# Optimization experiments

Measured on AMD Instinct MI355X. Metric: run time of the kernel, lower is better.

The kernel has to match this reference:

```python
import jax, jax.numpy as jnp
import numpy as np

DELTA = 0.2
TOPK = 10
RECALL_KS = (1, 5, 10)


def setup_inputs() -> dict:
    key = jax.random.key(0)
    k1, k2 = jax.random.split(key)
    B, D = 8192, 256
    x = jax.random.normal(k1, (B, D), dtype=jnp.float32)
    y = jax.random.normal(k2, (B, D), dtype=jnp.float32)
    return {"x": x, "y": y}


def reference(x, y):
    B = x.shape[0]
    # L2-normalize rows (matches x / sqrt(sum(x*x), keepdim))
    xn = x / jnp.sqrt(jnp.sum(x * x, axis=1, keepdims=True))
    yn = y / jnp.sqrt(jnp.sum(y * y, axis=1, keepdims=True))
    sim = xn @ yn.T                      # [B, B]
    diag = jnp.diagonal(sim)             # [B]
    cor = diag[:, None]                  # cor_similarity[i, j] = sim[i, i]
    loss_mat = jnp.maximum(0.0, sim - cor + DELTA) + jnp.maximum(0.0, sim.T - cor + DELTA)
    # zero the diagonal (vectorized version of the python loop)
    loss_mat = loss_mat * (1.0 - jnp.eye(B, dtype=loss_mat.dtype))
    loss = jnp.sum(loss_mat) / B

    # metrics (no grad in original)
    score = sim - cor                    # [B, B]
    _, pred = jax.lax.top_k(score, TOPK)  # [B, 10] indices, descending
    # torch code: pred.t() [10,B] eq arange(B); equivalent untransposed:
    correct = pred == jnp.arange(B)[:, None]          # [B, 10]
    correct_per_rank = jnp.sum(correct, axis=0)        # [10] hits at rank j
    recall = jnp.stack([jnp.sum(correct[:, :k]) for k in RECALL_KS]).astype(jnp.int32)
    # ndcg weight ln(2)/ln(2+j) for rank j (0-based), matching math.log(2)/math.log(2+j)
    w = jnp.log(2.0) / jnp.log(2.0 + jnp.arange(TOPK, dtype=jnp.float32))
    ndcg = jnp.stack([jnp.sum(correct_per_rank[:k].astype(jnp.float32) * w[:k]) for k in RECALL_KS])
    return loss, recall, ndcg
```

## Files before the change

### kernel.cpp

```cpp
#include <hip/hip_runtime.h>
#include <math.h>

#define NB 8192
#define ND 256
#define DELTA_F 0.2f

typedef __attribute__((ext_vector_type(8))) __bf16 bf16x8;
typedef __attribute__((ext_vector_type(4))) __bf16 bf16x4;
typedef __attribute__((ext_vector_type(4))) float f32x4;

__device__ __forceinline__ void gload16(const void* g, void* l) {
  __builtin_amdgcn_global_load_lds(
      (const __attribute__((address_space(1))) void*)g,
      (__attribute__((address_space(3))) void*)l, 16, 0, 0);
}

__global__ __launch_bounds__(256) void normalize_split_k(
    const float* __restrict__ x, const float* __restrict__ y,
    __bf16* __restrict__ Xh, __bf16* __restrict__ Xl,
    __bf16* __restrict__ Yh, __bf16* __restrict__ Yl,
    float* __restrict__ dd) {
  const int w = threadIdx.x >> 6, lane = threadIdx.x & 63;
  const int i = blockIdx.x * 4 + w;
  const size_t rbase = (size_t)i * ND;
  const float4 xv = *(const float4*)&x[rbase + lane * 4];
  const float4 yv = *(const float4*)&y[rbase + lane * 4];
  float sxx = xv.x * xv.x + xv.y * xv.y + xv.z * xv.z + xv.w * xv.w;
  float syy = yv.x * yv.x + yv.y * yv.y + yv.z * yv.z + yv.w * yv.w;
  float sxy = xv.x * yv.x + xv.y * yv.y + xv.z * yv.z + xv.w * yv.w;
#pragma unroll
  for (int o = 1; o < 64; o <<= 1) {
    sxx += __shfl_xor(sxx, o, 64);
    syy += __shfl_xor(syy, o, 64);
    sxy += __shfl_xor(sxy, o, 64);
  }
  const float ix = 1.0f / sqrtf(sxx);
  const float iy = 1.0f / sqrtf(syy);
  if (lane == 0) dd[i] = sxy * ix * iy;

  const float xs[4] = {xv.x * ix, xv.y * ix, xv.z * ix, xv.w * ix};
  const float ys[4] = {yv.x * iy, yv.y * iy, yv.z * iy, yv.w * iy};
  bf16x4 xh, xl, yh, yl;
#pragma unroll
  for (int e = 0; e < 4; ++e) {
    const __bf16 h = (__bf16)xs[e];
    xh[e] = h; xl[e] = (__bf16)(xs[e] - (float)h);
    const __bf16 g = (__bf16)ys[e];
    yh[e] = g; yl[e] = (__bf16)(ys[e] - (float)g);
  }
  *(bf16x4*)&Xh[rbase + lane * 4] = xh;
  *(bf16x4*)&Xl[rbase + lane * 4] = xl;
  *(bf16x4*)&Yh[rbase + lane * 4] = yh;
  *(bf16x4*)&Yl[rbase + lane * 4] = yl;
}

__global__ __launch_bounds__(256) void gemm_mfma(
    const __bf16* __restrict__ Xh, const __bf16* __restrict__ Xl,
    const __bf16* __restrict__ Yh, const __bf16* __restrict__ Yl,
    const float* __restrict__ dd,
    float* __restrict__ loss_accum, int* __restrict__ cnt) {
  __shared__ __bf16 sT[4][128][32];
  __shared__ int c_loc[128];
  __shared__ float lred[4];

  const int tid = threadIdx.x;
  const int lin = blockIdx.y * 64 + blockIdx.x;
  const int swz = (lin & 7) * 512 + (lin >> 3);
  const int bi = swz >> 6, bj = swz & 63;
  const int row0 = bi * 128, col0 = bj * 128;

  const int lane = tid & 63, wid = tid >> 6;
  const int wr = wid >> 1, wc = wid & 1;
  const int lr = lane & 15, lkc = lane >> 4;

  for (int r = tid; r < 128; r += 256) c_loc[r] = 0;

  const __bf16* msrc = (wid == 0) ? Xh : (wid == 1) ? Xl : (wid == 2) ? Yh : Yl;
  const int mbase = (wid < 2) ? row0 : col0;
  const int sr = lane >> 2, sc = lane & 3;
  const int ssw = sc ^ ((sr >> 1) & 3);
  const char* gp[8];
#pragma unroll
  for (int i = 0; i < 8; ++i)
    gp[i] = (const char*)msrc + (size_t)(mbase + i * 16 + sr) * (ND * 2) + ssw * 16;
  __bf16* const lbase = &sT[wid][0][0];

  f32x4 acc[4][4];
#pragma unroll
  for (int m = 0; m < 4; ++m)
#pragma unroll
    for (int n = 0; n < 4; ++n) acc[m][n] = (f32x4)(0.0f);

  const int arow = wr * 64 + lr;
  const int bcol = wc * 64 + lr;
  const int cko = (lkc ^ ((lr >> 1) & 3)) * 8;

#pragma unroll
  for (int k0 = 0; k0 < ND; k0 += 32) {
    __syncthreads();
#pragma unroll
    for (int i = 0; i < 8; ++i)
      gload16(gp[i] + k0 * 2, lbase + i * 512);
    __syncthreads();

    bf16x8 ah[4], al[4], bh[4], bl[4];
#pragma unroll
    for (int m = 0; m < 4; ++m) {
      ah[m] = *(const bf16x8*)&sT[0][arow + m * 16][cko];
      al[m] = *(const bf16x8*)&sT[1][arow + m * 16][cko];
    }
#pragma unroll
    for (int n = 0; n < 4; ++n) {
      bh[n] = *(const bf16x8*)&sT[2][bcol + n * 16][cko];
      bl[n] = *(const bf16x8*)&sT[3][bcol + n * 16][cko];
    }
#pragma unroll
    for (int m = 0; m < 4; ++m)
#pragma unroll
      for (int n = 0; n < 4; ++n) {
        acc[m][n] = __builtin_amdgcn_mfma_f32_16x16x32_bf16(ah[m], bh[n], acc[m][n], 0, 0, 0);
        acc[m][n] = __builtin_amdgcn_mfma_f32_16x16x32_bf16(ah[m], bl[n], acc[m][n], 0, 0, 0);
        acc[m][n] = __builtin_amdgcn_mfma_f32_16x16x32_bf16(al[m], bh[n], acc[m][n], 0, 0, 0);
      }
  }

  float djv[4];
#pragma unroll
  for (int n = 0; n < 4; ++n) djv[n] = dd[col0 + wc * 64 + n * 16 + lr];

  float lsum = 0.f;
#pragma unroll
  for (int m = 0; m < 4; ++m) {
    const int rbase = wr * 64 + m * 16 + lkc * 4;
#pragma unroll
    for (int q = 0; q < 4; ++q) {
      const int gi = row0 + rbase + q;
      const float dival = dd[gi];
      int cl = 0;
#pragma unroll
      for (int n = 0; n < 4; ++n) {
        const int gj = col0 + wc * 64 + n * 16 + lr;
        const float s = acc[m][n][q];
        if (gi != gj) {
          lsum += fmaxf(0.f, s - dival + DELTA_F) + fmaxf(0.f, s - djv[n] + DELTA_F);
          cl += (s > dival) ? 1 : 0;
        }
      }
      cl += __shfl_xor(cl, 1, 64);
      cl += __shfl_xor(cl, 2, 64);
      cl += __shfl_xor(cl, 4, 64);
      cl += __shfl_xor(cl, 8, 64);
      if (lr == 0) atomicAdd(&c_loc[rbase + q], cl);
    }
  }

#pragma unroll
  for (int o = 32; o > 0; o >>= 1) lsum += __shfl_down(lsum, o, 64);
  if (lane == 0) lred[wid] = lsum;
  __syncthreads();
  if (tid == 0) atomicAdd(loss_accum, lred[0] + lred[1] + lred[2] + lred[3]);
  if (tid < 128) atomicAdd(&cnt[row0 + tid], c_loc[tid]);
}

__global__ __launch_bounds__(256) void finalize_k(
    const float* __restrict__ loss_accum, const int* __restrict__ cnt,
    float* __restrict__ out) {
  const int t = threadIdx.x;
  float a6[6] = {0.f, 0.f, 0.f, 0.f, 0.f, 0.f};
  for (int i = t; i < NB; i += 256) {
    const int c = cnt[i];
    if (c < 10) {
      const float w = 0.69314718055994531f / logf(2.0f + (float)c);
      a6[2] += 1.f; a6[5] += w;
      if (c < 5) { a6[1] += 1.f; a6[4] += w; }
      if (c < 1) { a6[0] += 1.f; a6[3] += w; }
    }
  }
  __shared__ float red[6][4];
#pragma unroll
  for (int j = 0; j < 6; ++j) {
    float v = a6[j];
#pragma unroll
    for (int o = 32; o > 0; o >>= 1) v += __shfl_down(v, o, 64);
    if ((t & 63) == 0) red[j][t >> 6] = v;
  }
  __syncthreads();
  if (t == 0) {
    out[0] = loss_accum[0] / (float)NB;
#pragma unroll
    for (int j = 0; j < 6; ++j)
      out[1 + j] = red[j][0] + red[j][1] + red[j][2] + red[j][3];
  }
}

extern "C" void kernel_launch(void* const* d_in, const int* in_sizes, int n_in,
                              void* d_out, int out_size, void* d_ws, size_t ws_size,
                              hipStream_t stream) {
  const float* x = (const float*)d_in[0];
  const float* y = (const float*)d_in[1];
  float* out = (float*)d_out;

  char* ws = (char*)d_ws;
  float* loss_accum = (float*)ws;
  int* cnt = (int*)(ws + 256);
  float* dd = (float*)(ws + 256 + 32768);

  const size_t splitOff = 256 + 2 * 32768;
  const size_t matB = (size_t)NB * ND * 2;
  __bf16* Xh = (__bf16*)(ws + splitOff);
  __bf16* Xl = (__bf16*)(ws + splitOff + matB);
  __bf16* Yh = (__bf16*)(ws + splitOff + 2 * matB);
  __bf16* Yl = (__bf16*)(ws + splitOff + 3 * matB);

  hipMemsetAsync(ws, 0, 256 + 32768, stream);
  hipLaunchKernelGGL(normalize_split_k, dim3(NB / 4), dim3(256), 0, stream,
                     x, y, Xh, Xl, Yh, Yl, dd);
  hipLaunchKernelGGL(gemm_mfma, dim3(64, 64), dim3(256), 0, stream,
                     Xh, Xl, Yh, Yl, dd, loss_accum, cnt);
  hipLaunchKernelGGL(finalize_k, dim3(1), dim3(256), 0, stream, loss_accum, cnt, out);
}
```

Baseline: 155.0 us.

## Use 256x256 tiles with a 4-stage pipelined LDS loop over the split-bf16 K

```diff
diff --git a/kernel.cpp b/kernel.cpp
--- a/kernel.cpp
+++ b/kernel.cpp
@@ -4,6 +4,7 @@
 #define NB 8192
 #define ND 256
 #define DELTA_F 0.2f
+#define NT 24
 
 typedef __attribute__((ext_vector_type(8))) __bf16 bf16x8;
 typedef __attribute__((ext_vector_type(4))) __bf16 bf16x4;
@@ -19,7 +20,7 @@
     const float* __restrict__ x, const float* __restrict__ y,
     __bf16* __restrict__ Xh, __bf16* __restrict__ Xl,
     __bf16* __restrict__ Yh, __bf16* __restrict__ Yl,
-    float* __restrict__ dd) {
+    float* __restrict__ dd, float* __restrict__ loss_accum, int* __restrict__ cnt) {
   const int w = threadIdx.x >> 6, lane = threadIdx.x & 63;
   const int i = blockIdx.x * 4 + w;
   const size_t rbase = (size_t)i * ND;
@@ -36,8 +37,11 @@
   }
   const float ix = 1.0f / sqrtf(sxx);
   const float iy = 1.0f / sqrtf(syy);
-  if (lane == 0) dd[i] = sxy * ix * iy;
-
+  if (lane == 0) {
+    dd[i] = sxy * ix * iy;
+    cnt[i] = 0;
+    if (i == 0) loss_accum[0] = 0.0f;
+  }
   const float xs[4] = {xv.x * ix, xv.y * ix, xv.z * ix, xv.w * ix};
   const float ys[4] = {yv.x * iy, yv.y * iy, yv.z * iy, yv.w * iy};
   bf16x4 xh, xl, yh, yl;
@@ -54,74 +58,89 @@
   *(bf16x4*)&Yl[rbase + lane * 4] = yl;
 }
 
-__global__ __launch_bounds__(256) void gemm_mfma(
+__global__ __launch_bounds__(512, 2) void gemm_mfma(
     const __bf16* __restrict__ Xh, const __bf16* __restrict__ Xl,
     const __bf16* __restrict__ Yh, const __bf16* __restrict__ Yl,
     const float* __restrict__ dd,
     float* __restrict__ loss_accum, int* __restrict__ cnt) {
-  __shared__ __bf16 sT[4][128][32];
-  __shared__ int c_loc[128];
-  __shared__ float lred[4];
+  __shared__ __bf16 sAB[4][2][256][32];
+  __shared__ int c_loc[256];
+  __shared__ float lred[8];
 
   const int tid = threadIdx.x;
-  const int lin = blockIdx.y * 64 + blockIdx.x;
-  const int swz = (lin & 7) * 512 + (lin >> 3);
-  const int bi = swz >> 6, bj = swz & 63;
-  const int row0 = bi * 128, col0 = bj * 128;
+  const int bid = blockIdx.x;
+  const int xcd = bid & 7, idx = bid >> 3;
+  const int bi = xcd * 4 + (idx & 3);
+  const int bj = (idx >> 5) * 8 + ((idx >> 2) & 7);
+  const int row0 = bi * 256, col0 = bj * 256;
 
   const int lane = tid & 63, wid = tid >> 6;
-  const int wr = wid >> 1, wc = wid & 1;
+  const int wr = wid >> 2, wc = wid & 3;
   const int lr = lane & 15, lkc = lane >> 4;
 
-  for (int r = tid; r < 128; r += 256) c_loc[r] = 0;
-
-  const __bf16* msrc = (wid == 0) ? Xh : (wid == 1) ? Xl : (wid == 2) ? Yh : Yl;
-  const int mbase = (wid < 2) ? row0 : col0;
-  const int sr = lane >> 2, sc = lane & 3;
-  const int ssw = sc ^ ((sr >> 1) & 3);
-  const char* gp[8];
-#pragma unroll
-  for (int i = 0; i < 8; ++i)
-    gp[i] = (const char*)msrc + (size_t)(mbase + i * 16 + sr) * (ND * 2) + ssw * 16;
-  __bf16* const lbase = &sT[wid][0][0];
-
-  f32x4 acc[4][4];
-#pragma unroll
-  for (int m = 0; m < 4; ++m)
+  if (tid < 256) c_loc[tid] = 0;
+
+  const int rowl = tid >> 2;
+  const int swz = (tid & 3) ^ ((tid >> 3) & 3);
+  const size_t offA0 = (size_t)(row0 + rowl) * (ND * 2) + swz * 16;
+  const size_t offB0 = (size_t)(col0 + rowl) * (ND * 2) + swz * 16;
+  char* const lds0 = (char*)&sAB[0][0][0][0];
+
+  f32x4 acc[8][4];
+#pragma unroll
+  for (int m = 0; m < 8; ++m)
 #pragma unroll
     for (int n = 0; n < 4; ++n) acc[m][n] = (f32x4)(0.0f);
 
-  const int arow = wr * 64 + lr;
-  const int bcol = wc * 64 + lr;
+  auto stage = [&](int t) {
+    const char* pa = (const char*)((t >= 8 && t < 16) ? Xl : Xh) + (t & 7) * 64;
+    const char* pb = (const char*)((t >= 16) ? Yl : Yh) + (t & 7) * 64;
+    char* lb = lds0 + (t & 3) * 32768;
+    gload16(pa + offA0,         lb + tid * 16);
+    gload16(pa + offA0 + 65536, lb + 8192 + tid * 16);
+    gload16(pb + offB0,         lb + 16384 + tid * 16);
+    gload16(pb + offB0 + 65536, lb + 24576 + tid * 16);
+  };
+
   const int cko = (lkc ^ ((lr >> 1) & 3)) * 8;
-
-#pragma unroll
-  for (int k0 = 0; k0 < ND; k0 += 32) {
-    __syncthreads();
-#pragma unroll
-    for (int i = 0; i < 8; ++i)
-      gload16(gp[i] + k0 * 2, lbase + i * 512);
-    __syncthreads();
-
-    bf16x8 ah[4], al[4], bh[4], bl[4];
-#pragma unroll
-    for (int m = 0; m < 4; ++m) {
-      ah[m] = *(const bf16x8*)&sT[0][arow + m * 16][cko];
-      al[m] = *(const bf16x8*)&sT[1][arow + m * 16][cko];
-    }
-#pragma unroll
-    for (int n = 0; n < 4; ++n) {
-      bh[n] = *(const bf16x8*)&sT[2][bcol + n * 16][cko];
-      bl[n] = *(const bf16x8*)&sT[3][bcol + n * 16][cko];
-    }
+  const int arow = wr * 128 + lr;
+  const int brow = wc * 64 + lr;
+
+#pragma unroll
+  for (int t = 0; t < 3; ++t) stage(t);
+
+#pragma unroll
+  for (int t = 0; t < NT; ++t) {
+    if (t + 3 < NT) stage(t + 3);
+    __builtin_amdgcn_sched_barrier(0);
+    if (t < NT - 3)       asm volatile("s_waitcnt vmcnt(12)\n\ts_barrier" ::: "memory");
+    else if (t == NT - 3) asm volatile("s_waitcnt vmcnt(8)\n\ts_barrier" ::: "memory");
+    else if (t == NT - 2) asm volatile("s_waitcnt vmcnt(4)\n\ts_barrier" ::: "memory");
+    else                  asm volatile("s_waitcnt vmcnt(0)\n\ts_barrier" ::: "memory");
+
+    const int b = t & 3;
+    bf16x8 bf[4], af[8];
+#pragma unroll
+    for (int n = 0; n < 4; ++n) bf[n] = *(const bf16x8*)&sAB[b][1][brow + n * 16][cko];
+#pragma unroll
+    for (int m = 0; m < 8; ++m) af[m] = *(const bf16x8*)&sAB[b][0][arow + m * 16][cko];
+
+    __builtin_amdgcn_s_setprio(1);
 #pragma unroll
     for (int m = 0; m < 4; ++m)
 #pragma unroll
-      for (int n = 0; n < 4; ++n) {
-        acc[m][n] = __builtin_amdgcn_mfma_f32_16x16x32_bf16(ah[m], bh[n], acc[m][n], 0, 0, 0);
-        acc[m][n] = __builtin_amdgcn_mfma_f32_16x16x32_bf16(ah[m], bl[n], acc[m][n], 0, 0, 0);
-        acc[m][n] = __builtin_amdgcn_mfma_f32_16x16x32_bf16(al[m], bh[n], acc[m][n], 0, 0, 0);
-      }
+      for (int n = 0; n < 4; ++n)
+        acc[m][n] = __builtin_amdgcn_mfma_f32_16x16x32_bf16(af[m], bf[n], acc[m][n], 0, 0, 0);
+    __builtin_amdgcn_s_setprio(0);
+    asm volatile("s_barrier" ::: "memory");
+    __builtin_amdgcn_s_setprio(1);
+#pragma unroll
+    for (int m = 4; m < 8; ++m)
+#pragma unroll
+      for (int n = 0; n < 4; ++n)
+        acc[m][n] = __builtin_amdgcn_mfma_f32_16x16x32_bf16(af[m], bf[n], acc[m][n], 0, 0, 0);
+    __builtin_amdgcn_s_setprio(0);
+    asm volatile("s_barrier" ::: "memory");
   }
 
   float djv[4];
@@ -130,8 +149,8 @@
 
   float lsum = 0.f;
 #pragma unroll
-  for (int m = 0; m < 4; ++m) {
-    const int rbase = wr * 64 + m * 16 + lkc * 4;
+  for (int m = 0; m < 8; ++m) {
+    const int rbase = wr * 128 + m * 16 + lkc * 4;
 #pragma unroll
     for (int q = 0; q < 4; ++q) {
       const int gi = row0 + rbase + q;
@@ -158,8 +177,13 @@
   for (int o = 32; o > 0; o >>= 1) lsum += __shfl_down(lsum, o, 64);
   if (lane == 0) lred[wid] = lsum;
   __syncthreads();
-  if (tid == 0) atomicAdd(loss_accum, lred[0] + lred[1] + lred[2] + lred[3]);
-  if (tid < 128) atomicAdd(&cnt[row0 + tid], c_loc[tid]);
+  if (tid == 0) {
+    float s = 0.f;
+#pragma unroll
+    for (int w = 0; w < 8; ++w) s += lred[w];
+    atomicAdd(loss_accum, s);
+  }
+  if (tid < 256) atomicAdd(&cnt[row0 + tid], c_loc[tid]);
 }
 
 __global__ __launch_bounds__(256) void finalize_k(
@@ -212,10 +236,9 @@
   __bf16* Yh = (__bf16*)(ws + splitOff + 2 * matB);
   __bf16* Yl = (__bf16*)(ws + splitOff + 3 * matB);
 
-  hipMemsetAsync(ws, 0, 256 + 32768, stream);
   hipLaunchKernelGGL(normalize_split_k, dim3(NB / 4), dim3(256), 0, stream,
-                     x, y, Xh, Xl, Yh, Yl, dd);
-  hipLaunchKernelGGL(gemm_mfma, dim3(64, 64), dim3(256), 0, stream,
+                     x, y, Xh, Xl, Yh, Yl, dd, loss_accum, cnt);
+  hipLaunchKernelGGL(gemm_mfma, dim3(1024), dim3(512), 0, stream,
                      Xh, Xl, Yh, Yl, dd, loss_accum, cnt);
   hipLaunchKernelGGL(finalize_k, dim3(1), dim3(256), 0, stream, loss_accum, cnt, out);
 }
```

Result: slower. 168.2 us (+8.5%).
